# Optimization experiments

Measured on AMD Instinct MI355X. Metric: run time of the kernel, lower is better.

The kernel has to match this reference:

```python
import jax, jax.numpy as jnp
import numpy as np

N_NODES = 50000
N_EDGES = 800000
D = 64
N_LAYERS = 3  # zip(convs(4), batchnorms(3)) truncates to 3 executed layers
N_GRAPHS = 32
EPS_BN = 1e-5
NEG_SLOPE = 0.2


def segment_softmax(logits, seg, n):
    m = jax.ops.segment_max(logits, seg, num_segments=n)
    m = jnp.where(jnp.isfinite(m), m, 0.0)
    z = jnp.exp(logits - m[seg])
    s = jax.ops.segment_sum(z, seg, num_segments=n)
    return z / (s[seg] + 1e-16)


def setup_inputs() -> dict:
    key = jax.random.key(0)
    ks = jax.random.split(key, 16)
    s = 0.1
    return {
        "x": jax.random.normal(ks[0], (N_NODES, D), jnp.float32),
        "edge_index": jax.random.randint(ks[1], (2, N_EDGES), 0, N_NODES),
        "edge_attr": jax.random.normal(ks[2], (N_EDGES, D), jnp.float32),
        "batch": jnp.sort(jax.random.randint(ks[3], (N_NODES,), 0, N_GRAPHS)),
        # EdgeConvLayer MLP params (stacked over layers)
        "em_w1": jax.random.normal(ks[4], (N_LAYERS, 3 * D, D)) * s,
        "em_b1": jnp.zeros((N_LAYERS, D)),
        "em_w2": jax.random.normal(ks[5], (N_LAYERS, D, D)) * s,
        "em_b2": jnp.zeros((N_LAYERS, D)),
        # GATConv params (heads=1, add_self_loops=False)
        "gat_w": jax.random.normal(ks[6], (N_LAYERS, D, D)) * s,
        "att_src": jax.random.normal(ks[7], (N_LAYERS, D)) * s,
        "att_dst": jax.random.normal(ks[8], (N_LAYERS, D)) * s,
        "edge_w": jax.random.normal(ks[9], (N_LAYERS, D, D)) * s,
        "att_edge": jax.random.normal(ks[10], (N_LAYERS, D)) * s,
        "gat_bias": jnp.zeros((N_LAYERS, D)),
        # BatchNorm params
        "bn_gamma": jnp.ones((N_LAYERS, D)),
        "bn_beta": jnp.zeros((N_LAYERS, D)),
        # readout MLP
        "mlp_w1": jax.random.normal(ks[11], (D, D)) * s,
        "mlp_b1": jnp.zeros((D,)),
        "mlp_w2": jax.random.normal(ks[12], (D, D // 2)) * s,
        "mlp_b2": jnp.zeros((D // 2,)),
        "mlp_w3": jax.random.normal(ks[13], (D // 2, 1)) * s,
        "mlp_b3": jnp.zeros((1,)),
    }


def reference(x, edge_index, edge_attr, batch, em_w1, em_b1, em_w2, em_b2,
              gat_w, att_src, att_dst, edge_w, att_edge, gat_bias,
              bn_gamma, bn_beta, mlp_w1, mlp_b1, mlp_w2, mlp_b2, mlp_w3, mlp_b3):
    row, col = edge_index[0], edge_index[1]
    n = x.shape[0]
    for l in range(N_LAYERS):
        # MetaLayer edge model: cat(src, dst, edge_attr) -> 2-layer MLP
        cat = jnp.concatenate([x[row], x[col], edge_attr], axis=1)  # (E, 3D)
        eh = jax.nn.relu(cat @ em_w1[l] + em_b1[l])
        edge_attr = eh @ em_w2[l] + em_b2[l]  # (E, D)
        # GATConv, heads=1: shared linear for src/dst
        xw = x @ gat_w[l]  # (N, D)
        a_edge = edge_attr @ (edge_w[l] @ att_edge[l])  # fused lin_edge + att_edge dot
        logits = (xw @ att_src[l])[row] + (xw @ att_dst[l])[col] + a_edge
        alpha = segment_softmax(jax.nn.leaky_relu(logits, NEG_SLOPE), col, n)
        h = jax.ops.segment_sum(alpha[:, None] * xw[row], col, num_segments=n) + gat_bias[l]
        # BatchNorm (training batch stats) + ReLU
        mu = h.mean(axis=0)
        var = h.var(axis=0)
        x = jax.nn.relu((h - mu) * jax.lax.rsqrt(var + EPS_BN) * bn_gamma[l] + bn_beta[l])
    # global mean pool over graphs
    sums = jax.ops.segment_sum(x, batch, num_segments=N_GRAPHS)
    cnt = jax.ops.segment_sum(jnp.ones((n,), x.dtype), batch, num_segments=N_GRAPHS)
    g = sums / jnp.maximum(cnt, 1.0)[:, None]
    h = jax.nn.relu(g @ mlp_w1 + mlp_b1)
    h = jax.nn.relu(h @ mlp_w2 + mlp_b2)
    return h @ mlp_w3 + mlp_b3  # (N_GRAPHS, 1)
```

## Files before the change

kernel.cpp:

```cpp
#include <hip/hip_runtime.h>


#define NN 50000
#define NE 800000
#define NEG_SLOPE 0.2f

typedef __attribute__((ext_vector_type(8))) __bf16 bf16x8;
typedef __attribute__((ext_vector_type(4))) float f32x4;

__device__ __forceinline__ float4 ld4(const float* __restrict__ p){ return *(const float4* __restrict__)p; }
__device__ __forceinline__ float4 f4zero(){ return make_float4(0.f,0.f,0.f,0.f); }
__device__ __forceinline__ bf16x8 cvt8(float4 a, float4 b){
  bf16x8 r;
  r[0]=(__bf16)a.x; r[1]=(__bf16)a.y; r[2]=(__bf16)a.z; r[3]=(__bf16)a.w;
  r[4]=(__bf16)b.x; r[5]=(__bf16)b.y; r[6]=(__bf16)b.z; r[7]=(__bf16)b.w;
  return r;
}
__device__ __forceinline__ bf16x8 addpack8(bf16x8 a, bf16x8 b){
  bf16x8 r;
#pragma unroll
  for (int e = 0; e < 8; ++e) r[e] = (__bf16)((float)a[e] + (float)b[e]);
  return r;
}
__device__ __forceinline__ float4 bnrelu4(float4 v, const float* sc, const float* sh, int d){
  return make_float4(
    fmaxf(fmaf(v.x, sc[d+0], sh[d+0]), 0.f),
    fmaxf(fmaf(v.y, sc[d+1], sh[d+1]), 0.f),
    fmaxf(fmaf(v.z, sc[d+2], sh[d+2]), 0.f),
    fmaxf(fmaf(v.w, sc[d+3], sh[d+3]), 0.f));
}

__global__ __launch_bounds__(256) void setup_kernel(
    const int* __restrict__ ei_col, int* __restrict__ cnt,
    const int* __restrict__ batch, int* __restrict__ goff,
    const float* __restrict__ em_w1, const float* __restrict__ em_w2,
    const float* __restrict__ gat_w,
    const float* __restrict__ edge_w, const float* __restrict__ att_edge,
    __bf16* __restrict__ w1f, __bf16* __restrict__ w2f, __bf16* __restrict__ wnf,
    float* __restrict__ vbuf)
{
  const int b = blockIdx.x, t = threadIdx.x;
  if (b < NE/256){
    atomicAdd(&cnt[ei_col[b*256 + t]], 1);
    int n = b*256 + t;
    if (n < NN){
      int bn = batch[n];
      int bp = (n == 0) ? -1 : batch[n-1];
      for (int g = bp + 1; g <= bn; ++g) goff[g] = n;
      if (n == NN - 1){ for (int g = bn + 1; g <= 32; ++g) goff[g] = NN; }
    }
  } else {
    const int l = b - NE/256;
    const float* W1c = em_w1 + l*12288 + 8192;
    const float* W2  = em_w2 + l*4096;
    for (int p = t; p < 512; p += 256){
      int li = p & 63, ks = (p >> 6) & 1, nt = p >> 7;
      int kbase = ks*32 + (li >> 4)*8;
      int j = nt*16 + (li & 15);
      bf16x8 v1, v2;
#pragma unroll
      for (int e = 0; e < 8; ++e){
        v1[e] = (__bf16)W1c[(size_t)(kbase+e)*64 + j];
        v2[e] = (__bf16)W2[(size_t)(kbase+e)*64 + j];
      }
      *(bf16x8*)(w1f + (size_t)l*4096 + p*8) = v1;
      *(bf16x8*)(w2f + (size_t)l*4096 + p*8) = v2;
    }
    for (int pp = t; pp < 1536; pp += 256){
      int p = pp >> 9, piece = pp & 511;
      int li = piece & 63, ks = (piece >> 6) & 1, nt = piece >> 7;
      int kbase = ks*32 + (li >> 4)*8;
      int j = nt*16 + (li & 15);
      const float* W = (p == 0) ? (em_w1 + l*12288)
                     : (p == 1) ? (em_w1 + l*12288 + 4096)
                                : (gat_w + l*4096);
      bf16x8 v;
#pragma unroll
      for (int e = 0; e < 8; ++e) v[e] = (__bf16)W[(size_t)(kbase+e)*64 + j];
      *(bf16x8*)(wnf + (size_t)l*12288 + (size_t)p*4096 + piece*8) = v;
    }
    if (t < 64){
      float a = 0.f;
      const float* ew = edge_w + l*4096 + t*64;
      const float* ae = att_edge + l*64;
#pragma unroll 8
      for (int j = 0; j < 64; ++j) a = fmaf(ew[j], ae[j], a);
      vbuf[l*64 + t] = a;
    }
  }
}

__global__ __launch_bounds__(1024) void scan_kernel(const int* __restrict__ cnt,
                                                    int* __restrict__ off){
  __shared__ int wsum[16];
  __shared__ int carry_s;
  const int t = threadIdx.x;
  const int lane = t & 63, w = t >> 6;
  if (t == 0) carry_s = 0;
  __syncthreads();
  for (int base = 0; base < NN; base += 1024){
    int idx = base + t;
    int v = (idx < NN) ? cnt[idx] : 0;
    int x = v;
#pragma unroll
    for (int o = 1; o < 64; o <<= 1){
      int u = __shfl_up(x, o);
      if (lane >= o) x += u;
    }
    if (lane == 63) wsum[w] = x;
    __syncthreads();
    int wo = carry_s;
#pragma unroll
    for (int k = 0; k < 16; ++k) if (k < w) wo += wsum[k];
    int incl = x + wo;
    if (idx < NN) off[idx] = incl - v;
    __syncthreads();
    if (t == 1023) carry_s = incl;
    __syncthreads();
  }
  if (t == 0) off[NN] = carry_s;
}

__global__ __launch_bounds__(256) void scatter_kernel(
    const int* __restrict__ ei, const int* __restrict__ off, int* __restrict__ cur,
    int* __restrict__ srow, int* __restrict__ scol, int* __restrict__ perm){
  int e = blockIdx.x * 256 + threadIdx.x;
  int r = ei[e], c = ei[NE + e];
  int pos = off[c] + atomicAdd(&cur[c], 1);
  srow[pos] = r; scol[pos] = c; perm[pos] = e;
}

__global__ __launch_bounds__(256) void node_prep(
    const float* __restrict__ x0_in, const float* __restrict__ h_in,
    const float* __restrict__ bnpart,
    const float* __restrict__ gamma, const float* __restrict__ beta,
    const __bf16* __restrict__ wnf_l,
    const float* __restrict__ b1v,
    const float* __restrict__ asrc_g, const float* __restrict__ adst_g,
    __bf16* __restrict__ xaH, __bf16* __restrict__ xbH, __bf16* __restrict__ xwH,
    float* __restrict__ ssrc, float* __restrict__ sdst, int l)
{
  __shared__ __align__(16) __bf16 xf[64*72];
  __shared__ float sc[64], sh[64];
  __shared__ float b1s[64], asrc[64], adst[64];
  const int t = threadIdx.x;
  const int n0 = blockIdx.x * 64;
  const int w = t >> 6, lane = t & 63, m = lane & 15, kg = lane >> 4;

  if (l > 0){
    if (t < 64){
      float s = 0.f, s2 = 0.f;
#pragma unroll 8
      for (int k = 0; k < 64; ++k){
        s  += bnpart[k*128 + t];
        s2 += bnpart[k*128 + 64 + t];
      }
      float mu  = s * (1.0f / NN);
      float var = s2 * (1.0f / NN) - mu * mu;
      float iv  = rsqrtf(var + 1e-5f) * gamma[(l-1)*64 + t];
      sc[t] = iv;
      sh[t] = beta[(l-1)*64 + t] - mu * iv;
    }
    __syncthreads();
  }
  if (t < 64) b1s[t] = b1v[t];
  else if (t < 128) asrc[t-64] = asrc_g[t-64];
  else if (t < 192) adst[t-128] = adst_g[t-128];

  {
    const int e_loc = t >> 2, q = t & 3;
    const int n = n0 + e_loc;
    float4 v0, v1, v2, v3;
    if (n < NN){
      const float* src = ((l == 0) ? x0_in : h_in) + (size_t)n*64 + q*16;
      v0 = ld4(src); v1 = ld4(src+4); v2 = ld4(src+8); v3 = ld4(src+12);
      if (l > 0){
        v0 = bnrelu4(v0, sc, sh, q*16);
        v1 = bnrelu4(v1, sc, sh, q*16+4);
        v2 = bnrelu4(v2, sc, sh, q*16+8);
        v3 = bnrelu4(v3, sc, sh, q*16+12);
      }
    } else { v0 = v1 = v2 = v3 = f4zero(); }
    *(bf16x8*)&xf[e_loc*72 + q*16]     = cvt8(v0, v1);
    *(bf16x8*)&xf[e_loc*72 + q*16 + 8] = cvt8(v2, v3);
  }
  __syncthreads();

  const bf16x8 a0 = *(const bf16x8*)&xf[(16*w + m)*72 + kg*8];
  const bf16x8 a1 = *(const bf16x8*)&xf[(16*w + m)*72 + kg*8 + 32];
  const f32x4 z4 = {0.f, 0.f, 0.f, 0.f};

#pragma unroll
  for (int p = 0; p < 3; ++p){
    const bf16x8* Bp = (const bf16x8*)(wnf_l + (size_t)p*4096);
    f32x4 acc[4];
#pragma unroll
    for (int nt = 0; nt < 4; ++nt){
      acc[nt] = __builtin_amdgcn_mfma_f32_16x16x32_bf16(a0, Bp[(nt*2+0)*64 + lane], z4, 0, 0, 0);
      acc[nt] = __builtin_amdgcn_mfma_f32_16x16x32_bf16(a1, Bp[(nt*2+1)*64 + lane], acc[nt], 0, 0, 0);
    }
    __bf16* op = (p == 0) ? xaH : (p == 1) ? xbH : xwH;
#pragma unroll
    for (int nt = 0; nt < 4; ++nt){
      const int j = nt*16 + m;
      const float bb = (p == 0) ? b1s[j] : 0.f;
#pragma unroll
      for (int r = 0; r < 4; ++r){
        float v = acc[nt][r] + bb;
        unsigned short hu = __builtin_bit_cast(unsigned short, (__bf16)v);
        int pu = __shfl_xor((int)hu, 1);
        if (!(m & 1)){
          const int n = n0 + 16*w + 4*kg + r;
          if (n < NN){
            unsigned word = (unsigned)hu | ((unsigned)(pu & 0xffff) << 16);
            *(unsigned*)(op + (size_t)n*64 + (j & ~1)) = word;
          }
        }
      }
    }
    if (p == 2){
#pragma unroll
      for (int r = 0; r < 4; ++r){
        float s1 = 0.f, s2 = 0.f;
#pragma unroll
        for (int nt = 0; nt < 4; ++nt){
          s1 = fmaf(acc[nt][r], asrc[nt*16 + m], s1);
          s2 = fmaf(acc[nt][r], adst[nt*16 + m], s2);
        }
#pragma unroll
        for (int o = 8; o; o >>= 1){
          s1 += __shfl_xor(s1, o);
          s2 += __shfl_xor(s2, o);
        }
        if (m == 0){
          const int n = n0 + 16*w + 4*kg + r;
          if (n < NN){ ssrc[n] = s1; sdst[n] = s2; }
        }
      }
    }
  }
}

__global__ __launch_bounds__(256) void edge_mlp(
    const float* __restrict__ ea0,
    const __bf16* ea_in,
    __bf16* ea_out,
    const __bf16* __restrict__ xaH, const __bf16* __restrict__ xbH,
    const float* __restrict__ ssrc, const float* __restrict__ sdst,
    const int* __restrict__ srow, const int* __restrict__ scol,
    const int* __restrict__ permp,
    const __bf16* __restrict__ w1f, const __bf16* __restrict__ w2f,
    const float* __restrict__ b2v, const float* __restrict__ vv,
    float* __restrict__ lrelu, int store_ea)
{
  __shared__ __align__(16) __bf16 uvh[64*72];
  __shared__ __align__(16) unsigned ehw[2048];
  __shared__ float b2s[64], vs[64], sb[128];
  __shared__ int rs[128], cs[128], ps[128];
  const int t = threadIdx.x;
  const int w = t >> 6, l = t & 63, m = l & 15, kg = l >> 4;
  const int eb = blockIdx.x * 128;

  if (t < 128){ rs[t] = srow[eb+t]; cs[t] = scol[eb+t]; }
  else if (t < 192){ b2s[t-128] = b2v[t-128]; vs[t-128] = vv[t-128]; }
  if (permp && t < 128) ps[t] = permp[eb+t];
  __syncthreads();

  const bf16x8* B1 = (const bf16x8*)w1f;
  const bf16x8* B2 = (const bf16x8*)w2f;
  const f32x4 z4 = {0.f, 0.f, 0.f, 0.f};
  const int e_loc = t >> 2, q = t & 3;

  const int r0 = rs[e_loc],      c0 = cs[e_loc];
  const int r1 = rs[64 + e_loc], c1 = cs[64 + e_loc];
  const bf16x8* pa0 = (const bf16x8*)(xaH + (size_t)r0*64 + q*16);
  const bf16x8* pb0 = (const bf16x8*)(xbH + (size_t)c0*64 + q*16);
  const bf16x8* pa1 = (const bf16x8*)(xaH + (size_t)r1*64 + q*16);
  const bf16x8* pb1 = (const bf16x8*)(xbH + (size_t)c1*64 + q*16);
  bf16x8 g_a0l = pa0[0], g_a0h = pa0[1], g_b0l = pb0[0], g_b0h = pb0[1];
  bf16x8 g_a1l = pa1[0], g_a1h = pa1[1], g_b1l = pb1[0], g_b1h = pb1[1];
  float sb0 = 0.f, sb1 = 0.f;
  if (q == 0){ sb0 = ssrc[r0] + sdst[c0]; sb1 = ssrc[r1] + sdst[c1]; }

  bf16x8 A00, A01, A10, A11;
  { const int elA = 16*w + m;
    if (ea0){
      const float* s0 = ea0 + (size_t)ps[elA]*64 + kg*8;
      const float* s1 = ea0 + (size_t)ps[64+elA]*64 + kg*8;
      A00 = cvt8(ld4(s0),    ld4(s0+4));  A01 = cvt8(ld4(s0+32), ld4(s0+36));
      A10 = cvt8(ld4(s1),    ld4(s1+4));  A11 = cvt8(ld4(s1+32), ld4(s1+36));
    } else {
      const __bf16* s0 = ea_in + (size_t)(eb+elA)*64 + kg*8;
      const __bf16* s1 = ea_in + (size_t)(eb+64+elA)*64 + kg*8;
      A00 = *(const bf16x8*)s0;  A01 = *(const bf16x8*)(s0+32);
      A10 = *(const bf16x8*)s1;  A11 = *(const bf16x8*)(s1+32);
    }
  }

  *(bf16x8*)&uvh[e_loc*72 + q*16]     = addpack8(g_a0l, g_b0l);
  *(bf16x8*)&uvh[e_loc*72 + q*16 + 8] = addpack8(g_a0h, g_b0h);
  if (q == 0){ sb[e_loc] = sb0; sb[64 + e_loc] = sb1; }
  asm volatile("" ::: "memory");

  __bf16* esc = (__bf16*)ehw;
  auto tile_compute = [&](bf16x8 a0, bf16x8 a1, int tb){
    f32x4 acc[4];
#pragma unroll
    for (int nt = 0; nt < 4; ++nt){
      acc[nt] = __builtin_amdgcn_mfma_f32_16x16x32_bf16(a0, B1[(nt*2+0)*64 + l], z4, 0, 0, 0);
      acc[nt] = __builtin_amdgcn_mfma_f32_16x16x32_bf16(a1, B1[(nt*2+1)*64 + l], acc[nt], 0, 0, 0);
    }
#pragma unroll
    for (int nt = 0; nt < 4; ++nt){
      const int j = nt*16 + m;
#pragma unroll
      for (int r = 0; r < 4; ++r){
        const int erow = 16*w + 4*kg + r;
        float v = acc[nt][r] + (float)uvh[erow*72 + j];
        v = fmaxf(v, 0.f);
        const int piece = (w*2 + (nt>>1))*64 + (((nt&1)<<1) | (m>>3))*16 + 4*kg + r;
        esc[piece*8 + (m&7)] = (__bf16)v;
      }
    }
    asm volatile("" ::: "memory");
    bf16x8 a20 = *(const bf16x8*)(esc + (size_t)((w*2+0)*64 + kg*16 + m)*8);
    bf16x8 a21 = *(const bf16x8*)(esc + (size_t)((w*2+1)*64 + kg*16 + m)*8);
    f32x4 acc2[4];
#pragma unroll
    for (int nt = 0; nt < 4; ++nt){
      acc2[nt] = __builtin_amdgcn_mfma_f32_16x16x32_bf16(a20, B2[(nt*2+0)*64 + l], z4, 0, 0, 0);
      acc2[nt] = __builtin_amdgcn_mfma_f32_16x16x32_bf16(a21, B2[(nt*2+1)*64 + l], acc2[nt], 0, 0, 0);
    }
    float p0 = 0.f, p1 = 0.f, p2 = 0.f, p3 = 0.f;
#pragma unroll
    for (int nt = 0; nt < 4; ++nt){
      const int j = nt*16 + m;
      const float bj = b2s[j], vj = vs[j];
      float vr[4];
      vr[0] = acc2[nt][0] + bj; vr[1] = acc2[nt][1] + bj;
      vr[2] = acc2[nt][2] + bj; vr[3] = acc2[nt][3] + bj;
      if (store_ea){
        const size_t rowb = (size_t)(eb + tb + 16*w + 4*kg)*64 + (j & ~1);
#pragma unroll
        for (int r = 0; r < 4; ++r){
          unsigned short hu = __builtin_bit_cast(unsigned short, (__bf16)vr[r]);
          int pu = __shfl_xor((int)hu, 1);
          if (!(m & 1)){
            unsigned word = (unsigned)hu | ((unsigned)(pu & 0xffff) << 16);
            *(unsigned*)(ea_out + rowb + (size_t)r*64) = word;
          }
        }
      }
      p0 = fmaf(vr[0], vj, p0); p1 = fmaf(vr[1], vj, p1);
      p2 = fmaf(vr[2], vj, p2); p3 = fmaf(vr[3], vj, p3);
    }
#pragma unroll
    for (int o = 8; o; o >>= 1){
      p0 += __shfl_xor(p0, o); p1 += __shfl_xor(p1, o);
      p2 += __shfl_xor(p2, o); p3 += __shfl_xor(p3, o);
    }
    if (m == 0){
      float pv[4] = {p0, p1, p2, p3};
#pragma unroll
      for (int r = 0; r < 4; ++r){
        const int erow = 16*w + 4*kg + r;
        float logit = sb[tb + erow] + pv[r];
        lrelu[eb + tb + erow] = logit > 0.f ? logit : NEG_SLOPE * logit;
      }
    }
  };

  tile_compute(A00, A01, 0);
  asm volatile("" ::: "memory");
  *(bf16x8*)&uvh[e_loc*72 + q*16]     = addpack8(g_a1l, g_b1l);
  *(bf16x8*)&uvh[e_loc*72 + q*16 + 8] = addpack8(g_a1h, g_b1h);
  asm volatile("" ::: "memory");
  tile_compute(A10, A11, 64);
}

__global__ __launch_bounds__(256) void col_agg(
    const float* __restrict__ lrelu, const int* __restrict__ srow,
    const int* __restrict__ off, const __bf16* __restrict__ xwH,
    float* __restrict__ h)
{
  __shared__ float zS[4][128];
  __shared__ int   rS[4][128];
  const int t = threadIdx.x;
  const int lane = t & 63;
  const int wv = t >> 6;
  const int c = blockIdx.x * 4 + wv;
  const int s0 = off[c], s1 = off[c+1];
  const int L = s1 - s0;

  float l0 = (lane < L)    ? lrelu[s0+lane]    : -3.402823466e38f;
  float l1 = (lane+64 < L) ? lrelu[s0+64+lane] : -3.402823466e38f;
  int   r0 = (lane < L)    ? srow[s0+lane]     : 0;
  int   r1 = (lane+64 < L) ? srow[s0+64+lane]  : 0;

  float m = fmaxf(l0, l1);
  for (int i = lane+128; i < L; i += 64) m = fmaxf(m, lrelu[s0+i]);
#pragma unroll
  for (int o = 32; o; o >>= 1) m = fmaxf(m, __shfl_xor(m, o));

  float z0 = (lane < L)    ? expf(l0 - m) : 0.f;
  float z1 = (lane+64 < L) ? expf(l1 - m) : 0.f;
  float s = z0 + z1;
  for (int i = lane+128; i < L; i += 64) s += expf(lrelu[s0+i] - m);
#pragma unroll
  for (int o = 32; o; o >>= 1) s += __shfl_xor(s, o);
  const float inv = 1.f / (s + 1e-16f);

  zS[wv][lane] = z0;  zS[wv][64+lane] = z1;
  rS[wv][lane] = r0;  rS[wv][64+lane] = r1;
  asm volatile("" ::: "memory");

  float hv0 = 0.f, hv1 = 0.f, hv2 = 0.f, hv3 = 0.f;
  float hv4 = 0.f, hv5 = 0.f, hv6 = 0.f, hv7 = 0.f;
  if (L <= 128){
    int i = 0;
    for (; i + 8 <= L; i += 8){
      float za = zS[wv][i],   zb = zS[wv][i+1], zc = zS[wv][i+2], zd = zS[wv][i+3];
      float ze = zS[wv][i+4], zf = zS[wv][i+5], zg = zS[wv][i+6], zh = zS[wv][i+7];
      int   ra = rS[wv][i],   rb = rS[wv][i+1], rc = rS[wv][i+2], rd = rS[wv][i+3];
      int   re = rS[wv][i+4], rf = rS[wv][i+5], rg = rS[wv][i+6], rh = rS[wv][i+7];
      hv0 = fmaf(za, (float)xwH[(size_t)ra*64 + lane], hv0);
      hv1 = fmaf(zb, (float)xwH[(size_t)rb*64 + lane], hv1);
      hv2 = fmaf(zc, (float)xwH[(size_t)rc*64 + lane], hv2);
      hv3 = fmaf(zd, (float)xwH[(size_t)rd*64 + lane], hv3);
      hv4 = fmaf(ze, (float)xwH[(size_t)re*64 + lane], hv4);
      hv5 = fmaf(zf, (float)xwH[(size_t)rf*64 + lane], hv5);
      hv6 = fmaf(zg, (float)xwH[(size_t)rg*64 + lane], hv6);
      hv7 = fmaf(zh, (float)xwH[(size_t)rh*64 + lane], hv7);
    }
    for (; i < L; ++i)
      hv0 = fmaf(zS[wv][i], (float)xwH[(size_t)rS[wv][i]*64 + lane], hv0);
  } else {
    for (int i = 0; i < L; ++i){
      float z = expf(lrelu[s0+i] - m);
      int r = srow[s0+i];
      hv0 = fmaf(z, (float)xwH[(size_t)r*64 + lane], hv0);
    }
  }
  float hv = ((hv0 + hv1) + (hv2 + hv3)) + ((hv4 + hv5) + (hv6 + hv7));
  h[(size_t)c*64 + lane] = hv * inv;
}

__global__ __launch_bounds__(256) void bn_stats(
    const float* __restrict__ h, float* __restrict__ bnpart)
{
  const int g = blockIdx.x;
  const int t = threadIdx.x;
  const int d = t & 63, sub = t >> 6;
  const int n0 = g * 782;
  const int n1 = (n0 + 782 < NN) ? n0 + 782 : NN;
  float s = 0.f, s2 = 0.f;
  for (int n = n0 + sub; n < n1; n += 4){
    float v = h[(size_t)n*64 + d];
    s += v; s2 = fmaf(v, v, s2);
  }
  __shared__ float r1[4][64], r2[4][64];
  r1[sub][d] = s; r2[sub][d] = s2;
  __syncthreads();
  if (sub == 0){
    s  = r1[0][d] + r1[1][d] + r1[2][d] + r1[3][d];
    s2 = r2[0][d] + r2[1][d] + r2[2][d] + r2[3][d];
    bnpart[g*128 + d]      = s;
    bnpart[g*128 + 64 + d] = s2;
  }
}

__global__ __launch_bounds__(256) void seg_pool(
    const float* __restrict__ h, const int* __restrict__ goff,
    const float* __restrict__ bnpart,
    const float* __restrict__ gamma2, const float* __restrict__ beta2,
    float* __restrict__ pools, float* __restrict__ pcnt)
{
  __shared__ float sc[64], sh[64];
  const int g = blockIdx.x;
  const int t = threadIdx.x;
  const int d = t & 63, sub = t >> 6;
  if (t < 64){
    float s = 0.f, s2 = 0.f;
#pragma unroll 8
    for (int k = 0; k < 64; ++k){
      s  += bnpart[k*128 + t];
      s2 += bnpart[k*128 + 64 + t];
    }
    float mu  = s * (1.0f / NN);
    float var = s2 * (1.0f / NN) - mu * mu;
    float iv  = rsqrtf(var + 1e-5f) * gamma2[t];
    sc[t] = iv;
    sh[t] = beta2[t] - mu * iv;
  }
  __syncthreads();
  const int s0 = goff[g], s1 = goff[g+1];
  float s = 0.f;
  for (int n = s0 + sub; n < s1; n += 4)
    s += fmaxf(fmaf(h[(size_t)n*64 + d], sc[d], sh[d]), 0.f);
  __shared__ float r[4][64];
  r[sub][d] = s;
  __syncthreads();
  if (sub == 0){
    s = r[0][d] + r[1][d] + r[2][d] + r[3][d];
    pools[g*64 + d] = s;
    if (d == 0) pcnt[g] = (float)(s1 - s0);
  }
}

__global__ __launch_bounds__(256) void final_mlp(
    const float* __restrict__ pools, const float* __restrict__ pcnt,
    const float* __restrict__ w1, const float* __restrict__ b1,
    const float* __restrict__ w2, const float* __restrict__ b2,
    const float* __restrict__ w3, const float* __restrict__ b3,
    float* __restrict__ out)
{
  __shared__ float g[32*64], h1[32*64], h2[32*32];
  const int t = threadIdx.x;
  for (int i = t; i < 2048; i += 256) g[i] = pools[i] / fmaxf(pcnt[i >> 6], 1.0f);
  __syncthreads();
  for (int i = t; i < 2048; i += 256){
    int gi = i >> 6, d = i & 63;
    float a = b1[d];
    for (int k = 0; k < 64; ++k) a = fmaf(g[gi*64 + k], w1[k*64 + d], a);
    h1[i] = fmaxf(a, 0.f);
  }
  __syncthreads();
  for (int i = t; i < 1024; i += 256){
    int gi = i >> 5, d = i & 31;
    float a = b2[d];
    for (int k = 0; k < 64; ++k) a = fmaf(h1[gi*64 + k], w2[k*32 + d], a);
    h2[i] = fmaxf(a, 0.f);
  }
  __syncthreads();
  if (t < 32){
    float a = b3[0];
    for (int k = 0; k < 32; ++k) a = fmaf(h2[t*32 + k], w3[k], a);
    out[t] = a;
  }
}

extern "C" void kernel_launch(void* const* d_in, const int* in_sizes, int n_in,
                              void* d_out, int out_size, void* d_ws, size_t ws_size,
                              hipStream_t stream)
{
  (void)in_sizes; (void)n_in; (void)out_size; (void)ws_size;
  const float* x0       = (const float*)d_in[0];
  const int*   ei       = (const int*)  d_in[1];
  const float* ea0      = (const float*)d_in[2];
  const int*   batch    = (const int*)  d_in[3];
  const float* em_w1    = (const float*)d_in[4];
  const float* em_b1    = (const float*)d_in[5];
  const float* em_w2    = (const float*)d_in[6];
  const float* em_b2    = (const float*)d_in[7];
  const float* gat_w    = (const float*)d_in[8];
  const float* att_src  = (const float*)d_in[9];
  const float* att_dst  = (const float*)d_in[10];
  const float* edge_w   = (const float*)d_in[11];
  const float* att_edge = (const float*)d_in[12];
  const float* bn_gamma = (const float*)d_in[14];
  const float* bn_beta  = (const float*)d_in[15];
  const float* mlp_w1   = (const float*)d_in[16];
  const float* mlp_b1   = (const float*)d_in[17];
  const float* mlp_w2   = (const float*)d_in[18];
  const float* mlp_b2   = (const float*)d_in[19];
  const float* mlp_w3   = (const float*)d_in[20];
  const float* mlp_b3   = (const float*)d_in[21];
  float* out = (float*)d_out;

  const size_t N64 = (size_t)NN * 64, E64 = (size_t)NE * 64;
  float* ws    = (float*)d_ws;
  float* wsE   = ws;
  float* sxa   = wsE + E64;
  float* sxb   = sxa + N64;
  float* sxw   = sxb + N64;
  float* hbuf  = sxw + N64;
  float* bnpart= hbuf + N64;
  float* lrelu = bnpart + 64*128;
  float* pools = lrelu + NE;
  float* pcnt  = pools + 2048;
  float* ssrc  = pcnt + 32;
  float* sdst  = ssrc + NN;
  int*   cnt   = (int*)(sdst + NN);
  int*   cur   = cnt + NN;
  int*   soff  = cur + NN;
  int*   srow  = soff + NN + 1;
  int*   scol  = srow + NE;
  int*   perm  = scol + NE;
  int*   goff  = perm + NE;
  __bf16* eaB  = (__bf16*)wsE;
  __bf16* xaH  = (__bf16*)sxa;
  __bf16* xbH  = (__bf16*)sxb;
  __bf16* xwH  = (__bf16*)sxw;
  __bf16* w1f  = (__bf16*)(goff + 40);
  __bf16* w2f  = w1f + 3*4096;
  __bf16* wnf  = w2f + 3*4096;
  float* vbuf  = (float*)(wnf + 3*12288);

  hipMemsetAsync(cnt, 0, 2 * NN * sizeof(int), stream);
  setup_kernel<<<NE/256 + 3, 256, 0, stream>>>(
      ei + NE, cnt, batch, goff, em_w1, em_w2, gat_w, edge_w, att_edge,
      w1f, w2f, wnf, vbuf);
  scan_kernel<<<1, 1024, 0, stream>>>(cnt, soff);
  scatter_kernel<<<NE / 256, 256, 0, stream>>>(ei, soff, cur, srow, scol, perm);

  for (int l = 0; l < 3; ++l){
    node_prep<<<(NN + 63) / 64, 256, 0, stream>>>(
        x0, hbuf, bnpart, bn_gamma, bn_beta,
        wnf + (size_t)l*12288, em_b1 + l*64, att_src + l*64, att_dst + l*64,
        xaH, xbH, xwH, ssrc, sdst, l);

    edge_mlp<<<NE / 128, 256, 0, stream>>>(
        (l == 0) ? ea0 : nullptr, eaB, eaB, xaH, xbH, ssrc, sdst,
        srow, scol, (l == 0) ? perm : nullptr,
        w1f + (size_t)l*4096, w2f + (size_t)l*4096,
        em_b2 + l*64, vbuf + l*64, lrelu, (l < 2) ? 1 : 0);

    col_agg<<<NN / 4, 256, 0, stream>>>(lrelu, srow, soff, xwH, hbuf);

    bn_stats<<<64, 256, 0, stream>>>(hbuf, bnpart);
  }

  seg_pool<<<32, 256, 0, stream>>>(hbuf, goff, bnpart,
                                   bn_gamma + 128, bn_beta + 128, pools, pcnt);
  final_mlp<<<1, 256, 0, stream>>>(pools, pcnt, mlp_w1, mlp_b1, mlp_w2, mlp_b2,
                                   mlp_w3, mlp_b3, out);
}
```

Measured before the change: 788.0 us.

## Interleave xa/xw rows, materialize edge-ordered xw in edge_mlp, parallelize scan

```diff
diff --git a/kernel.cpp b/kernel.cpp
--- a/kernel.cpp
+++ b/kernel.cpp
@@ -90,35 +90,54 @@
   }
 }
 
-__global__ __launch_bounds__(1024) void scan_kernel(const int* __restrict__ cnt,
-                                                    int* __restrict__ off){
-  __shared__ int wsum[16];
-  __shared__ int carry_s;
-  const int t = threadIdx.x;
+__global__ __launch_bounds__(256) void scanA(const int* __restrict__ cnt,
+                                             int* __restrict__ soff,
+                                             int* __restrict__ btot){
+  __shared__ int wsum[4];
+  const int b = blockIdx.x, t = threadIdx.x;
   const int lane = t & 63, w = t >> 6;
-  if (t == 0) carry_s = 0;
-  __syncthreads();
-  for (int base = 0; base < NN; base += 1024){
-    int idx = base + t;
-    int v = (idx < NN) ? cnt[idx] : 0;
-    int x = v;
-#pragma unroll
-    for (int o = 1; o < 64; o <<= 1){
-      int u = __shfl_up(x, o);
-      if (lane >= o) x += u;
-    }
-    if (lane == 63) wsum[w] = x;
-    __syncthreads();
-    int wo = carry_s;
-#pragma unroll
-    for (int k = 0; k < 16; ++k) if (k < w) wo += wsum[k];
-    int incl = x + wo;
-    if (idx < NN) off[idx] = incl - v;
-    __syncthreads();
-    if (t == 1023) carry_s = incl;
-    __syncthreads();
-  }
-  if (t == 0) off[NN] = carry_s;
+  int idx = b*256 + t;
+  int v = (idx < NN) ? cnt[idx] : 0;
+  int x = v;
+#pragma unroll
+  for (int o = 1; o < 64; o <<= 1){
+    int u = __shfl_up(x, o);
+    if (lane >= o) x += u;
+  }
+  if (lane == 63) wsum[w] = x;
+  __syncthreads();
+  int wo = 0;
+#pragma unroll
+  for (int k = 0; k < 4; ++k) if (k < w) wo += wsum[k];
+  int incl = x + wo;
+  if (idx < NN) soff[idx] = incl - v;
+  if (t == 255) btot[b] = incl;
+}
+__global__ __launch_bounds__(256) void scanB(const int* __restrict__ btot,
+                                             int* __restrict__ btotex,
+                                             int* __restrict__ soff){
+  __shared__ int wsum[4];
+  const int t = threadIdx.x, lane = t & 63, w = t >> 6;
+  int v = (t < 196) ? btot[t] : 0;
+  int x = v;
+#pragma unroll
+  for (int o = 1; o < 64; o <<= 1){
+    int u = __shfl_up(x, o);
+    if (lane >= o) x += u;
+  }
+  if (lane == 63) wsum[w] = x;
+  __syncthreads();
+  int wo = 0;
+#pragma unroll
+  for (int k = 0; k < 4; ++k) if (k < w) wo += wsum[k];
+  int incl = x + wo;
+  if (t < 196) btotex[t] = incl - v;
+  if (t == 195) soff[NN] = incl;
+}
+__global__ __launch_bounds__(256) void scanC(int* __restrict__ soff,
+                                             const int* __restrict__ btotex){
+  int idx = blockIdx.x*256 + threadIdx.x;
+  if (idx < NN) soff[idx] += btotex[blockIdx.x];
 }
 
 __global__ __launch_bounds__(256) void scatter_kernel(
@@ -137,7 +156,7 @@
     const __bf16* __restrict__ wnf_l,
     const float* __restrict__ b1v,
     const float* __restrict__ asrc_g, const float* __restrict__ adst_g,
-    __bf16* __restrict__ xaH, __bf16* __restrict__ xbH, __bf16* __restrict__ xwH,
+    __bf16* __restrict__ xrH, __bf16* __restrict__ xbH,
     float* __restrict__ ssrc, float* __restrict__ sdst, int l)
 {
   __shared__ __align__(16) __bf16 xf[64*72];
@@ -167,8 +186,7 @@
   else if (t < 128) asrc[t-64] = asrc_g[t-64];
   else if (t < 192) adst[t-128] = adst_g[t-128];
 
-  {
-    const int e_loc = t >> 2, q = t & 3;
+  { const int e_loc = t >> 2, q = t & 3;
     const int n = n0 + e_loc;
     float4 v0, v1, v2, v3;
     if (n < NN){
@@ -199,7 +217,9 @@
       acc[nt] = __builtin_amdgcn_mfma_f32_16x16x32_bf16(a0, Bp[(nt*2+0)*64 + lane], z4, 0, 0, 0);
       acc[nt] = __builtin_amdgcn_mfma_f32_16x16x32_bf16(a1, Bp[(nt*2+1)*64 + lane], acc[nt], 0, 0, 0);
     }
-    __bf16* op = (p == 0) ? xaH : (p == 1) ? xbH : xwH;
+    __bf16* base = (p == 1) ? xbH : xrH;
+    const int stride = (p == 1) ? 64 : 128;
+    const int off0 = (p == 2) ? 64 : 0;
 #pragma unroll
     for (int nt = 0; nt < 4; ++nt){
       const int j = nt*16 + m;
@@ -213,7 +233,7 @@
           const int n = n0 + 16*w + 4*kg + r;
           if (n < NN){
             unsigned word = (unsigned)hu | ((unsigned)(pu & 0xffff) << 16);
-            *(unsigned*)(op + (size_t)n*64 + (j & ~1)) = word;
+            *(unsigned*)(base + (size_t)n*stride + off0 + (j & ~1)) = word;
           }
         }
       }
@@ -243,9 +263,9 @@
 
 __global__ __launch_bounds__(256) void edge_mlp(
     const float* __restrict__ ea0,
-    const __bf16* ea_in,
-    __bf16* ea_out,
-    const __bf16* __restrict__ xaH, const __bf16* __restrict__ xbH,
+    const __bf16* ea_in, __bf16* ea_out,
+    const __bf16* __restrict__ xrH, const __bf16* __restrict__ xbH,
+    __bf16* __restrict__ xwe,
     const float* __restrict__ ssrc, const float* __restrict__ sdst,
     const int* __restrict__ srow, const int* __restrict__ scol,
     const int* __restrict__ permp,
@@ -273,12 +293,14 @@
 
   const int r0 = rs[e_loc],      c0 = cs[e_loc];
   const int r1 = rs[64 + e_loc], c1 = cs[64 + e_loc];
-  const bf16x8* pa0 = (const bf16x8*)(xaH + (size_t)r0*64 + q*16);
+  const bf16x8* pr0 = (const bf16x8*)(xrH + (size_t)r0*128 + q*16);
   const bf16x8* pb0 = (const bf16x8*)(xbH + (size_t)c0*64 + q*16);
-  const bf16x8* pa1 = (const bf16x8*)(xaH + (size_t)r1*64 + q*16);
+  const bf16x8* pr1 = (const bf16x8*)(xrH + (size_t)r1*128 + q*16);
   const bf16x8* pb1 = (const bf16x8*)(xbH + (size_t)c1*64 + q*16);
-  bf16x8 g_a0l = pa0[0], g_a0h = pa0[1], g_b0l = pb0[0], g_b0h = pb0[1];
-  bf16x8 g_a1l = pa1[0], g_a1h = pa1[1], g_b1l = pb1[0], g_b1h = pb1[1];
+  bf16x8 g_a0l = pr0[0], g_a0h = pr0[1], g_b0l = pb0[0], g_b0h = pb0[1];
+  bf16x8 g_a1l = pr1[0], g_a1h = pr1[1], g_b1l = pb1[0], g_b1h = pb1[1];
+  bf16x8 w0l = pr0[8], w0h = pr0[9];
+  bf16x8 w1l = pr1[8], w1h = pr1[9];
   float sb0 = 0.f, sb1 = 0.f;
   if (q == 0){ sb0 = ssrc[r0] + sdst[c0]; sb1 = ssrc[r1] + sdst[c1]; }
 
@@ -297,6 +319,11 @@
     }
   }
 
+  { __bf16* d0 = xwe + (size_t)(eb + e_loc)*64 + q*16;
+    *(bf16x8*)d0 = w0l; *(bf16x8*)(d0+8) = w0h;
+    __bf16* d1 = xwe + (size_t)(eb + 64 + e_loc)*64 + q*16;
+    *(bf16x8*)d1 = w1l; *(bf16x8*)(d1+8) = w1h; }
+
   *(bf16x8*)&uvh[e_loc*72 + q*16]     = addpack8(g_a0l, g_b0l);
   *(bf16x8*)&uvh[e_loc*72 + q*16 + 8] = addpack8(g_a0h, g_b0h);
   if (q == 0){ sb[e_loc] = sb0; sb[64 + e_loc] = sb1; }
@@ -379,12 +406,10 @@
 }
 
 __global__ __launch_bounds__(256) void col_agg(
-    const float* __restrict__ lrelu, const int* __restrict__ srow,
-    const int* __restrict__ off, const __bf16* __restrict__ xwH,
-    float* __restrict__ h)
+    const float* __restrict__ lrelu, const int* __restrict__ off,
+    const __bf16* __restrict__ xwe, float* __restrict__ h)
 {
   __shared__ float zS[4][128];
-  __shared__ int   rS[4][128];
   const int t = threadIdx.x;
   const int lane = t & 63;
   const int wv = t >> 6;
@@ -394,8 +419,6 @@
 
   float l0 = (lane < L)    ? lrelu[s0+lane]    : -3.402823466e38f;
   float l1 = (lane+64 < L) ? lrelu[s0+64+lane] : -3.402823466e38f;
-  int   r0 = (lane < L)    ? srow[s0+lane]     : 0;
-  int   r1 = (lane+64 < L) ? srow[s0+64+lane]  : 0;
 
   float m = fmaxf(l0, l1);
   for (int i = lane+128; i < L; i += 64) m = fmaxf(m, lrelu[s0+i]);
@@ -411,34 +434,29 @@
   const float inv = 1.f / (s + 1e-16f);
 
   zS[wv][lane] = z0;  zS[wv][64+lane] = z1;
-  rS[wv][lane] = r0;  rS[wv][64+lane] = r1;
   asm volatile("" ::: "memory");
 
   float hv0 = 0.f, hv1 = 0.f, hv2 = 0.f, hv3 = 0.f;
   float hv4 = 0.f, hv5 = 0.f, hv6 = 0.f, hv7 = 0.f;
+  const __bf16* xp = xwe + (size_t)s0*64 + lane;
   if (L <= 128){
     int i = 0;
     for (; i + 8 <= L; i += 8){
-      float za = zS[wv][i],   zb = zS[wv][i+1], zc = zS[wv][i+2], zd = zS[wv][i+3];
-      float ze = zS[wv][i+4], zf = zS[wv][i+5], zg = zS[wv][i+6], zh = zS[wv][i+7];
-      int   ra = rS[wv][i],   rb = rS[wv][i+1], rc = rS[wv][i+2], rd = rS[wv][i+3];
-      int   re = rS[wv][i+4], rf = rS[wv][i+5], rg = rS[wv][i+6], rh = rS[wv][i+7];
-      hv0 = fmaf(za, (float)xwH[(size_t)ra*64 + lane], hv0);
-      hv1 = fmaf(zb, (float)xwH[(size_t)rb*64 + lane], hv1);
-      hv2 = fmaf(zc, (float)xwH[(size_t)rc*64 + lane], hv2);
-      hv3 = fmaf(zd, (float)xwH[(size_t)rd*64 + lane], hv3);
-      hv4 = fmaf(ze, (float)xwH[(size_t)re*64 + lane], hv4);
-      hv5 = fmaf(zf, (float)xwH[(size_t)rf*64 + lane], hv5);
-      hv6 = fmaf(zg, (float)xwH[(size_t)rg*64 + lane], hv6);
-      hv7 = fmaf(zh, (float)xwH[(size_t)rh*64 + lane], hv7);
+      hv0 = fmaf(zS[wv][i],   (float)xp[(size_t)(i  )*64], hv0);
+      hv1 = fmaf(zS[wv][i+1], (float)xp[(size_t)(i+1)*64], hv1);
+      hv2 = fmaf(zS[wv][i+2], (float)xp[(size_t)(i+2)*64], hv2);
+      hv3 = fmaf(zS[wv][i+3], (float)xp[(size_t)(i+3)*64], hv3);
+      hv4 = fmaf(zS[wv][i+4], (float)xp[(size_t)(i+4)*64], hv4);
+      hv5 = fmaf(zS[wv][i+5], (float)xp[(size_t)(i+5)*64], hv5);
+      hv6 = fmaf(zS[wv][i+6], (float)xp[(size_t)(i+6)*64], hv6);
+      hv7 = fmaf(zS[wv][i+7], (float)xp[(size_t)(i+7)*64], hv7);
     }
     for (; i < L; ++i)
-      hv0 = fmaf(zS[wv][i], (float)xwH[(size_t)rS[wv][i]*64 + lane], hv0);
+      hv0 = fmaf(zS[wv][i], (float)xp[(size_t)i*64], hv0);
   } else {
     for (int i = 0; i < L; ++i){
       float z = expf(lrelu[s0+i] - m);
-      int r = srow[s0+i];
-      hv0 = fmaf(z, (float)xwH[(size_t)r*64 + lane], hv0);
+      hv0 = fmaf(z, (float)xp[(size_t)i*64], hv0);
     }
   }
   float hv = ((hv0 + hv1) + (hv2 + hv3)) + ((hv4 + hv5) + (hv6 + hv7));
@@ -570,10 +588,9 @@
   const size_t N64 = (size_t)NN * 64, E64 = (size_t)NE * 64;
   float* ws    = (float*)d_ws;
   float* wsE   = ws;
-  float* sxa   = wsE + E64;
-  float* sxb   = sxa + N64;
-  float* sxw   = sxb + N64;
-  float* hbuf  = sxw + N64;
+  float* sxr   = wsE + E64;
+  float* sxb   = sxr + N64;
+  float* hbuf  = sxb + N64;
   float* bnpart= hbuf + N64;
   float* lrelu = bnpart + 64*128;
   float* pools = lrelu + NE;
@@ -587,11 +604,13 @@
   int*   scol  = srow + NE;
   int*   perm  = scol + NE;
   int*   goff  = perm + NE;
+  int*   btot  = goff + 40;
+  int*   btotex= btot + 256;
   __bf16* eaB  = (__bf16*)wsE;
-  __bf16* xaH  = (__bf16*)sxa;
+  __bf16* xwe  = (__bf16*)(wsE + E64/2);
+  __bf16* xrH  = (__bf16*)sxr;
   __bf16* xbH  = (__bf16*)sxb;
-  __bf16* xwH  = (__bf16*)sxw;
-  __bf16* w1f  = (__bf16*)(goff + 40);
+  __bf16* w1f  = (__bf16*)(btotex + 256);
   __bf16* w2f  = w1f + 3*4096;
   __bf16* wnf  = w2f + 3*4096;
   float* vbuf  = (float*)(wnf + 3*12288);
@@ -600,22 +619,24 @@
   setup_kernel<<<NE/256 + 3, 256, 0, stream>>>(
       ei + NE, cnt, batch, goff, em_w1, em_w2, gat_w, edge_w, att_edge,
       w1f, w2f, wnf, vbuf);
-  scan_kernel<<<1, 1024, 0, stream>>>(cnt, soff);
+  scanA<<<196, 256, 0, stream>>>(cnt, soff, btot);
+  scanB<<<1, 256, 0, stream>>>(btot, btotex, soff);
+  scanC<<<196, 256, 0, stream>>>(soff, btotex);
   scatter_kernel<<<NE / 256, 256, 0, stream>>>(ei, soff, cur, srow, scol, perm);
 
   for (int l = 0; l < 3; ++l){
     node_prep<<<(NN + 63) / 64, 256, 0, stream>>>(
         x0, hbuf, bnpart, bn_gamma, bn_beta,
         wnf + (size_t)l*12288, em_b1 + l*64, att_src + l*64, att_dst + l*64,
-        xaH, xbH, xwH, ssrc, sdst, l);
+        xrH, xbH, ssrc, sdst, l);
 
     edge_mlp<<<NE / 128, 256, 0, stream>>>(
-        (l == 0) ? ea0 : nullptr, eaB, eaB, xaH, xbH, ssrc, sdst,
+        (l == 0) ? ea0 : nullptr, eaB, eaB, xrH, xbH, xwe, ssrc, sdst,
         srow, scol, (l == 0) ? perm : nullptr,
         w1f + (size_t)l*4096, w2f + (size_t)l*4096,
         em_b2 + l*64, vbuf + l*64, lrelu, (l < 2) ? 1 : 0);
 
-    col_agg<<<NN / 4, 256, 0, stream>>>(lrelu, srow, soff, xwH, hbuf);
+    col_agg<<<NN / 4, 256, 0, stream>>>(lrelu, soff, xwe, hbuf);
 
     bn_stats<<<64, 256, 0, stream>>>(hbuf, bnpart);
   }
```

Result: slower. 829.7 us (+5.3%).
